# Optimization experiments

Measured on AMD Instinct MI355X. Metric: run time of the kernel, lower is better.

Reference implementation:

```python
import jax, jax.numpy as jnp
import numpy as np

EPS = 1e-12  # F.normalize eps
REGION = (5, 5)
STRIDE = (2, 2)


def _l2norm(v, axis):
    n = jnp.sqrt(jnp.sum(v * v, axis=axis, keepdims=True))
    return v / jnp.maximum(n, EPS)


def setup_inputs() -> dict:
    key = jax.random.key(0)
    k1, k2, k3 = jax.random.split(key, 3)
    N, C, H, W, K = 4, 128, 40, 40, 64
    x = jax.random.normal(k1, (N, C, H, W), dtype=jnp.float32)
    conv_w = jax.random.normal(k2, (K, C), dtype=jnp.float32)  # 1x1 conv, no bias (vladv2=False)
    centroids = jax.random.uniform(k3, (K, C), dtype=jnp.float32)  # torch.rand init
    return {"x": x, "conv_w": conv_w, "centroids": centroids}


def reference(x, conv_w, centroids):
    N, C, H, W = x.shape
    K = centroids.shape[0]
    # descriptor-wise L2 normalization over channels
    x = _l2norm(x, axis=1)
    # 1x1 conv -> soft assignment over clusters
    soft_assign = jnp.einsum('nchw,kc->nkhw', x, conv_w)
    soft_assign = jax.nn.softmax(soft_assign, axis=1)
    # soft-assign-weighted residuals: [N, K, C, H, W]
    resid = x[:, None, :, :, :] - centroids[None, :, :, None, None]
    store = resid * soft_assign[:, :, None, :, :]
    # global VLAD (sum over all spatial locations)
    vlad_full = store.sum(axis=(-1, -2))  # [N, K, C]
    # regional average pooling (kernel 5x5, stride 2, valid)
    Hout = (H - REGION[0]) // STRIDE[0] + 1
    Wout = (W - REGION[1]) // STRIDE[1] + 1
    pooled = jax.lax.reduce_window(
        store.reshape(N, K * C, H, W), 0.0, jax.lax.add,
        (1, 1, REGION[0], REGION[1]), (1, 1, STRIDE[0], STRIDE[1]), 'VALID')
    pooled = pooled / (REGION[0] * REGION[1])
    # regional VLAD: intra-norm over C, flatten, global L2 norm
    vlad = pooled.reshape(N, K, C, Hout, Wout)
    vlad = _l2norm(vlad, axis=2)
    vlad = vlad.reshape(N, K * C, Hout * Wout)
    vlad = _l2norm(vlad, axis=1)
    # full VLAD: intra-norm over C, flatten, global L2 norm
    vlad_full = _l2norm(vlad_full, axis=2)
    vlad_full = vlad_full.reshape(N, K * C)
    vlad_full = _l2norm(vlad_full, axis=1)
    return vlad, vlad_full
```

## Files before the change

kernel.cpp:

```cpp
#include <hip/hip_runtime.h>

#define EPSN 1e-12f

#define NB   4
#define CC   128
#define KK_  64
#define HH   40
#define WW   40
#define HWP  1600
#define HO   18
#define WO   18
#define HWO  324
#define KCC  8192

#define WS_XN  0
#define WS_A   819200
#define WS_GP  1228800
#define WS_G0  1753088

static __device__ __forceinline__ int swz(int c){ return c ^ ((c & 96) >> 3); }

__global__ __launch_bounds__(1024) void k1_norm_assign(
    const float* __restrict__ x, const float* __restrict__ w,
    float* __restrict__ xn, float* __restrict__ aout)
{
  __shared__ float xs[64][133];
  __shared__ float ds[64][65];
  __shared__ float invs[64];
  const int t = threadIdx.x;
  const int b = blockIdx.x;
  const int n = b / 25;
  const int pixb = (b % 25) * 64;
  const float* xb = x + (size_t)n * CC * HWP + pixb;

  {
    const int pix = t & 63, cs = t >> 6;
    #pragma unroll
    for (int j = 0; j < 8; ++j) {
      const int c = cs + 16 * j;
      xs[pix][c] = xb[c * HWP + pix];
    }
  }
  __syncthreads();
  {
    const int p = t >> 4, q = t & 15;
    float ss = 0.f;
    #pragma unroll
    for (int j = 0; j < 8; ++j) { float v = xs[p][q + 16 * j]; ss += v * v; }
    ss += __shfl_xor(ss, 1); ss += __shfl_xor(ss, 2);
    ss += __shfl_xor(ss, 4); ss += __shfl_xor(ss, 8);
    if (q == 0) invs[p] = 1.f / fmaxf(sqrtf(ss), EPSN);
  }
  __syncthreads();
  {
    float* xno = xn + ((size_t)n * HWP + pixb) * CC;
    #pragma unroll
    for (int rr = 0; rr < 8; ++rr) {
      const int i = t + rr * 1024;
      const int pp = i >> 7, c = i & 127;
      const float v = xs[pp][c] * invs[pp];
      xs[pp][c] = v;
      xno[i] = v;
    }
  }
  __syncthreads();
  {
    const int lane = t & 63;
    const int wv = __builtin_amdgcn_readfirstlane(t >> 6);
    float acc[4] = {0.f, 0.f, 0.f, 0.f};
    for (int c = 0; c < CC; ++c) {
      const float vn = xs[lane][c];
      #pragma unroll
      for (int kk = 0; kk < 4; ++kk)
        acc[kk] += vn * w[(wv * 4 + kk) * CC + c];
    }
    #pragma unroll
    for (int kk = 0; kk < 4; ++kk) ds[lane][wv * 4 + kk] = acc[kk];
  }
  __syncthreads();
  {
    const int p = t >> 4, q = t & 15;
    float v[4]; float m = -3.4e38f;
    #pragma unroll
    for (int kk = 0; kk < 4; ++kk){ v[kk] = ds[p][q + 16 * kk]; m = fmaxf(m, v[kk]); }
    m = fmaxf(m, __shfl_xor(m, 1)); m = fmaxf(m, __shfl_xor(m, 2));
    m = fmaxf(m, __shfl_xor(m, 4)); m = fmaxf(m, __shfl_xor(m, 8));
    float s = 0.f;
    #pragma unroll
    for (int kk = 0; kk < 4; ++kk){ v[kk] = __expf(v[kk] - m); s += v[kk]; }
    s += __shfl_xor(s, 1); s += __shfl_xor(s, 2);
    s += __shfl_xor(s, 4); s += __shfl_xor(s, 8);
    const float is = 1.f / s;
    #pragma unroll
    for (int kk = 0; kk < 4; ++kk) ds[p][q + 16 * kk] = v[kk] * is;
  }
  __syncthreads();
  {
    float* ao = aout + ((size_t)n * HWP + pixb) * KK_;
    #pragma unroll
    for (int rr = 0; rr < 4; ++rr) {
      const int i = t + rr * 1024;
      ao[i] = ds[i >> 6][i & 63];
    }
  }
}

__device__ __forceinline__ void dots25(const float (*a_s)[64], const float (*xs)[128],
                                       int k, int cg, float acc[32], float& s0)
{
  #pragma unroll
  for (int p = 0; p < 25; ++p) {
    const float av = a_s[p][k];
    s0 += av;
    #pragma unroll
    for (int m = 0; m < 8; ++m) {
      const float4 x4 = *(const float4*)&xs[p][(cg << 5) + ((m ^ cg) << 2)];
      acc[(m << 2) + 0] += av * x4.x;
      acc[(m << 2) + 1] += av * x4.y;
      acc[(m << 2) + 2] += av * x4.z;
      acc[(m << 2) + 3] += av * x4.w;
    }
  }
}

__global__ __launch_bounds__(256) void k2_main(
    const float* __restrict__ xn, const float* __restrict__ aw,
    const float* __restrict__ cent, float* __restrict__ out,
    float* __restrict__ Gpart, float* __restrict__ G0part)
{
  __shared__ __align__(16) float a_s[25][64];
  __shared__ __align__(16) float xs[25][128];
  __shared__ float red[4];
  const int t = threadIdx.x;
  const int lane = t & 63;
  const int wv = t >> 6;
  const int kq = lane >> 2;
  const int cg = lane & 3;
  const int k = wv * 16 + kq;
  const int bid = (blockIdx.x & 7) * 170 + (blockIdx.x >> 3);

  float acc[32];
  #pragma unroll
  for (int j = 0; j < 32; ++j) acc[j] = 0.f;
  float s0 = 0.f;

  if (bid < 1296) {
    const int n = bid / HWO, r = bid % HWO, ho = r / WO, wo = r % WO;
    for (int it = wv; it < 25; it += 4) {
      const int pix = (2 * ho + it / 5) * WW + 2 * wo + (it % 5);
      a_s[it][lane] = aw[((size_t)n * HWP + pix) * KK_ + lane];
      const float* xp = xn + ((size_t)n * HWP + pix) * CC;
      xs[it][swz(lane)]      = xp[lane];
      xs[it][swz(lane + 64)] = xp[lane + 64];
    }
    __syncthreads();

    dots25(a_s, xs, k, cg, acc, s0);

    float ss = 0.f;
    #pragma unroll
    for (int m = 0; m < 8; ++m) {
      const float4 c4 = *(const float4*)&cent[(size_t)k * CC + (cg << 5) + (m << 2)];
      const float cv[4] = {c4.x, c4.y, c4.z, c4.w};
      #pragma unroll
      for (int d = 0; d < 4; ++d) {
        const float pv = (acc[(m << 2) + d] - cv[d] * s0) * 0.04f;
        acc[(m << 2) + d] = pv;
        ss += pv * pv;
      }
    }
    ss += __shfl_xor(ss, 1); ss += __shfl_xor(ss, 2);
    const float rn = 1.f / fmaxf(sqrtf(ss), EPSN);
    float gp = (cg == 0) ? ss * rn * rn : 0.f;
    #pragma unroll
    for (int o = 1; o < 64; o <<= 1) gp += __shfl_xor(gp, o);
    if (lane == 0) red[wv] = gp;
    __syncthreads();
    const float gtot = red[0] + red[1] + red[2] + red[3];
    const float scale = rn * (1.f / fmaxf(sqrtf(gtot), EPSN));

    float* ob = out + (size_t)n * KCC * HWO + r;
    #pragma unroll
    for (int j = 0; j < 32; ++j)
      ob[(size_t)(k * CC + (cg << 5) + j) * HWO] = acc[j] * scale;
  } else {
    const int pid = bid - 1296;
    const int n = pid >> 4, ch = pid & 15;
    const int pixb = n * HWP + ch * 100;
    #pragma unroll 1
    for (int rr = 0; rr < 4; ++rr) {
      for (int it = wv; it < 25; it += 4) {
        const int pg = pixb + rr * 25 + it;
        a_s[it][lane] = aw[(size_t)pg * KK_ + lane];
        const float* xp = xn + (size_t)pg * CC;
        xs[it][swz(lane)]      = xp[lane];
        xs[it][swz(lane + 64)] = xp[lane + 64];
      }
      __syncthreads();
      dots25(a_s, xs, k, cg, acc, s0);
      __syncthreads();
    }
    if (cg == 0) G0part[(size_t)pid * KK_ + k] = s0;
    float* gb = Gpart + (size_t)pid * KCC + (size_t)k * CC + (cg << 5);
    #pragma unroll
    for (int m = 0; m < 8; ++m) {
      float4 v;
      v.x = acc[(m << 2) + 0]; v.y = acc[(m << 2) + 1];
      v.z = acc[(m << 2) + 2]; v.w = acc[(m << 2) + 3];
      *(float4*)&gb[m << 2] = v;
    }
  }
}

__global__ __launch_bounds__(1024) void k3_full(
    const float* __restrict__ Gpart, const float* __restrict__ G0part,
    const float* __restrict__ cent, float* __restrict__ outF)
{
  __shared__ float red[16];
  const int n = blockIdx.x;
  const int t = threadIdx.x;
  const int k = t >> 4, cg16 = t & 15;
  const int c0 = cg16 * 8;

  float acc[8];
  #pragma unroll
  for (int j = 0; j < 8; ++j) acc[j] = 0.f;
  float g0 = 0.f;
  #pragma unroll 1
  for (int ch = 0; ch < 16; ++ch) {
    const float* gp = Gpart + ((size_t)(n * 16 + ch)) * KCC + (size_t)k * CC + c0;
    const float4 a4 = *(const float4*)(gp);
    const float4 b4 = *(const float4*)(gp + 4);
    acc[0] += a4.x; acc[1] += a4.y; acc[2] += a4.z; acc[3] += a4.w;
    acc[4] += b4.x; acc[5] += b4.y; acc[6] += b4.z; acc[7] += b4.w;
    g0 += G0part[(size_t)(n * 16 + ch) * KK_ + k];
  }

  float ss = 0.f;
  #pragma unroll
  for (int j = 0; j < 8; ++j) {
    const float v = acc[j] - cent[(size_t)k * CC + c0 + j] * g0;
    acc[j] = v;
    ss += v * v;
  }
  ss += __shfl_xor(ss, 1); ss += __shfl_xor(ss, 2);
  ss += __shfl_xor(ss, 4); ss += __shfl_xor(ss, 8);
  const float rn = 1.f / fmaxf(sqrtf(ss), EPSN);
  float part = (cg16 == 0) ? ss * rn * rn : 0.f;
  #pragma unroll
  for (int o = 1; o < 64; o <<= 1) part += __shfl_xor(part, o);
  if ((t & 63) == 0) red[t >> 6] = part;
  __syncthreads();
  float tot = 0.f;
  #pragma unroll
  for (int i = 0; i < 16; ++i) tot += red[i];
  const float scale = rn * (1.f / fmaxf(sqrtf(tot), EPSN));
  #pragma unroll
  for (int j = 0; j < 8; ++j)
    outF[(size_t)n * KCC + (size_t)k * CC + c0 + j] = acc[j] * scale;
}

extern "C" void kernel_launch(void* const* d_in, const int* in_sizes, int n_in,
                              void* d_out, int out_size, void* d_ws, size_t ws_size,
                              hipStream_t stream)
{
  const float* x    = (const float*)d_in[0];
  const float* w    = (const float*)d_in[1];
  const float* cent = (const float*)d_in[2];
  float* out = (float*)d_out;
  float* ws  = (float*)d_ws;

  float* xn = ws + WS_XN;
  float* aw = ws + WS_A;
  float* gp = ws + WS_GP;
  float* g0 = ws + WS_G0;

  k1_norm_assign<<<dim3(100), dim3(1024), 0, stream>>>(x, w, xn, aw);
  k2_main<<<dim3(1360), dim3(256), 0, stream>>>(xn, aw, cent, out, gp, g0);
  k3_full<<<dim3(NB), dim3(1024), 0, stream>>>(gp, g0, cent,
                                               out + (size_t)NB * KCC * HWO);
}
```

Baseline: 156.9 us.

## Stage regional VLAD in coalesced scratch buffer and add transpose kernel

The main kernel now writes regional VLAD values to a workspace buffer laid out as [n, region, K*C] with float4 stores, instead of scattering single floats with a stride of HWO straight into the output. A new shared-memory tiled transpose kernel then moves the data into the required [n, K*C, region] output layout. Thread work is also remapped so each lane owns 4 channels across 8 clusters, which changes how the per-cluster norm reductions use shuffles. The aim is to replace strided, uncoalesced global writes, at the cost of an extra full write and read of the output-sized buffer plus one more kernel launch.

```diff
diff --git a/kernel.cpp b/kernel.cpp
--- a/kernel.cpp
+++ b/kernel.cpp
@@ -13,12 +13,11 @@
 #define HWO  324
 #define KCC  8192
 
-#define WS_XN  0
-#define WS_A   819200
-#define WS_GP  1228800
-#define WS_G0  1753088
-
-static __device__ __forceinline__ int swz(int c){ return c ^ ((c & 96) >> 3); }
+#define WS_T   0
+#define WS_XN  10616832
+#define WS_A   11436032
+#define WS_GP  11845632
+#define WS_G0  12369920
 
 __global__ __launch_bounds__(1024) void k1_norm_assign(
     const float* __restrict__ x, const float* __restrict__ w,
@@ -106,26 +105,27 @@
 }
 
 __device__ __forceinline__ void dots25(const float (*a_s)[64], const float (*xs)[128],
-                                       int k, int cg, float acc[32], float& s0)
+                                       int kbase, int h, int c0,
+                                       float acc[32], float s0[8])
 {
   #pragma unroll
   for (int p = 0; p < 25; ++p) {
-    const float av = a_s[p][k];
-    s0 += av;
-    #pragma unroll
-    for (int m = 0; m < 8; ++m) {
-      const float4 x4 = *(const float4*)&xs[p][(cg << 5) + ((m ^ cg) << 2)];
-      acc[(m << 2) + 0] += av * x4.x;
-      acc[(m << 2) + 1] += av * x4.y;
-      acc[(m << 2) + 2] += av * x4.z;
-      acc[(m << 2) + 3] += av * x4.w;
+    const float4 x4 = *(const float4*)&xs[p][c0];
+    #pragma unroll
+    for (int m = 0; m < 8; ++m) {
+      const float av = a_s[p][kbase + 2 * m + h];
+      s0[m] += av;
+      acc[m * 4 + 0] += av * x4.x;
+      acc[m * 4 + 1] += av * x4.y;
+      acc[m * 4 + 2] += av * x4.z;
+      acc[m * 4 + 3] += av * x4.w;
     }
   }
 }
 
 __global__ __launch_bounds__(256) void k2_main(
     const float* __restrict__ xn, const float* __restrict__ aw,
-    const float* __restrict__ cent, float* __restrict__ out,
+    const float* __restrict__ cent, float* __restrict__ T,
     float* __restrict__ Gpart, float* __restrict__ G0part)
 {
   __shared__ __align__(16) float a_s[25][64];
@@ -134,15 +134,18 @@
   const int t = threadIdx.x;
   const int lane = t & 63;
   const int wv = t >> 6;
-  const int kq = lane >> 2;
-  const int cg = lane & 3;
-  const int k = wv * 16 + kq;
+  const int h = lane >> 5;
+  const int l5 = lane & 31;
+  const int c0 = l5 << 2;
+  const int kbase = wv * 16;
   const int bid = (blockIdx.x & 7) * 170 + (blockIdx.x >> 3);
 
   float acc[32];
   #pragma unroll
   for (int j = 0; j < 32; ++j) acc[j] = 0.f;
-  float s0 = 0.f;
+  float s0[8];
+  #pragma unroll
+  for (int m = 0; m < 8; ++m) s0[m] = 0.f;
 
   if (bid < 1296) {
     const int n = bid / HWO, r = bid % HWO, ho = r / WO, wo = r % WO;
@@ -150,39 +153,54 @@
       const int pix = (2 * ho + it / 5) * WW + 2 * wo + (it % 5);
       a_s[it][lane] = aw[((size_t)n * HWP + pix) * KK_ + lane];
       const float* xp = xn + ((size_t)n * HWP + pix) * CC;
-      xs[it][swz(lane)]      = xp[lane];
-      xs[it][swz(lane + 64)] = xp[lane + 64];
+      xs[it][lane]      = xp[lane];
+      xs[it][lane + 64] = xp[lane + 64];
     }
     __syncthreads();
 
-    dots25(a_s, xs, k, cg, acc, s0);
-
-    float ss = 0.f;
-    #pragma unroll
-    for (int m = 0; m < 8; ++m) {
-      const float4 c4 = *(const float4*)&cent[(size_t)k * CC + (cg << 5) + (m << 2)];
+    dots25(a_s, xs, kbase, h, c0, acc, s0);
+
+    float ssm[8], rnm[8];
+    #pragma unroll
+    for (int m = 0; m < 8; ++m) {
+      const int k = kbase + 2 * m + h;
+      const float4 c4 = *(const float4*)&cent[(size_t)k * CC + c0];
       const float cv[4] = {c4.x, c4.y, c4.z, c4.w};
+      float ss = 0.f;
       #pragma unroll
       for (int d = 0; d < 4; ++d) {
-        const float pv = (acc[(m << 2) + d] - cv[d] * s0) * 0.04f;
-        acc[(m << 2) + d] = pv;
+        const float pv = (acc[m * 4 + d] - cv[d] * s0[m]) * 0.04f;
+        acc[m * 4 + d] = pv;
         ss += pv * pv;
       }
-    }
-    ss += __shfl_xor(ss, 1); ss += __shfl_xor(ss, 2);
-    const float rn = 1.f / fmaxf(sqrtf(ss), EPSN);
-    float gp = (cg == 0) ? ss * rn * rn : 0.f;
-    #pragma unroll
-    for (int o = 1; o < 64; o <<= 1) gp += __shfl_xor(gp, o);
-    if (lane == 0) red[wv] = gp;
+      ssm[m] = ss;
+    }
+    #pragma unroll
+    for (int off = 1; off <= 16; off <<= 1) {
+      #pragma unroll
+      for (int m = 0; m < 8; ++m) ssm[m] += __shfl_xor(ssm[m], off);
+    }
+    float gpl = 0.f;
+    #pragma unroll
+    for (int m = 0; m < 8; ++m) {
+      rnm[m] = 1.f / fmaxf(sqrtf(ssm[m]), EPSN);
+      gpl += ssm[m] * rnm[m] * rnm[m];
+    }
+    gpl += __shfl_xor(gpl, 32);
+    if (lane == 0) red[wv] = gpl;
     __syncthreads();
     const float gtot = red[0] + red[1] + red[2] + red[3];
-    const float scale = rn * (1.f / fmaxf(sqrtf(gtot), EPSN));
-
-    float* ob = out + (size_t)n * KCC * HWO + r;
-    #pragma unroll
-    for (int j = 0; j < 32; ++j)
-      ob[(size_t)(k * CC + (cg << 5) + j) * HWO] = acc[j] * scale;
+    const float gi = 1.f / fmaxf(sqrtf(gtot), EPSN);
+
+    float* tb = T + ((size_t)n * HWO + r) * KCC + kbase * CC;
+    #pragma unroll
+    for (int m = 0; m < 8; ++m) {
+      const float sc = rnm[m] * gi;
+      float4 v;
+      v.x = acc[m * 4 + 0] * sc; v.y = acc[m * 4 + 1] * sc;
+      v.z = acc[m * 4 + 2] * sc; v.w = acc[m * 4 + 3] * sc;
+      *(float4*)&tb[m * 256 + lane * 4] = v;
+    }
   } else {
     const int pid = bid - 1296;
     const int n = pid >> 4, ch = pid & 15;
@@ -193,22 +211,53 @@
         const int pg = pixb + rr * 25 + it;
         a_s[it][lane] = aw[(size_t)pg * KK_ + lane];
         const float* xp = xn + (size_t)pg * CC;
-        xs[it][swz(lane)]      = xp[lane];
-        xs[it][swz(lane + 64)] = xp[lane + 64];
+        xs[it][lane]      = xp[lane];
+        xs[it][lane + 64] = xp[lane + 64];
       }
       __syncthreads();
-      dots25(a_s, xs, k, cg, acc, s0);
+      dots25(a_s, xs, kbase, h, c0, acc, s0);
       __syncthreads();
     }
-    if (cg == 0) G0part[(size_t)pid * KK_ + k] = s0;
-    float* gb = Gpart + (size_t)pid * KCC + (size_t)k * CC + (cg << 5);
+    if (l5 == 0) {
+      #pragma unroll
+      for (int m = 0; m < 8; ++m)
+        G0part[(size_t)pid * KK_ + kbase + 2 * m + h] = s0[m];
+    }
+    float* gb = Gpart + (size_t)pid * KCC + kbase * CC;
     #pragma unroll
     for (int m = 0; m < 8; ++m) {
       float4 v;
-      v.x = acc[(m << 2) + 0]; v.y = acc[(m << 2) + 1];
-      v.z = acc[(m << 2) + 2]; v.w = acc[(m << 2) + 3];
-      *(float4*)&gb[m << 2] = v;
-    }
+      v.x = acc[m * 4 + 0]; v.y = acc[m * 4 + 1];
+      v.z = acc[m * 4 + 2]; v.w = acc[m * 4 + 3];
+      *(float4*)&gb[m * 256 + lane * 4] = v;
+    }
+  }
+}
+
+__global__ __launch_bounds__(256) void k4_transpose(
+    const float* __restrict__ T, float* __restrict__ out)
+{
+  __shared__ float tile[112][65];
+  const int t = threadIdx.x;
+  const int b = blockIdx.x;
+  const int n = b / 384;
+  const int rem = b % 384;
+  const int kcT = rem / 3, rT = rem % 3;
+  const int kc0 = kcT * 64;
+  const int r0 = rT * 112;
+  const int rows = (rT == 2) ? 100 : 112;
+  const int w = t >> 6, lane = t & 63;
+
+  for (int rr = w; rr < rows; rr += 4)
+    tile[rr][lane] = T[((size_t)n * HWO + r0 + rr) * KCC + kc0 + lane];
+  __syncthreads();
+
+  #pragma unroll
+  for (int j = 0; j < 16; ++j) {
+    const int kcl = w + 4 * j;
+    float* orow = out + (size_t)n * KCC * HWO + (size_t)(kc0 + kcl) * HWO + r0;
+    orow[lane] = tile[lane][kcl];
+    if (lane + 64 < rows) orow[64 + lane] = tile[64 + lane][kcl];
   }
 }
 
@@ -270,13 +319,15 @@
   float* out = (float*)d_out;
   float* ws  = (float*)d_ws;
 
+  float* T  = ws + WS_T;
   float* xn = ws + WS_XN;
   float* aw = ws + WS_A;
   float* gp = ws + WS_GP;
   float* g0 = ws + WS_G0;
 
   k1_norm_assign<<<dim3(100), dim3(1024), 0, stream>>>(x, w, xn, aw);
-  k2_main<<<dim3(1360), dim3(256), 0, stream>>>(xn, aw, cent, out, gp, g0);
+  k2_main<<<dim3(1360), dim3(256), 0, stream>>>(xn, aw, cent, T, gp, g0);
+  k4_transpose<<<dim3(1536), dim3(256), 0, stream>>>(T, out);
   k3_full<<<dim3(NB), dim3(1024), 0, stream>>>(gp, g0, cent,
                                                out + (size_t)NB * KCC * HWO);
 }
```

Measured after the change: 162.6 us. 3.6% more time.
